# Performance work log

Hardware: AMD Instinct MI355X
Metric: run time of the kernel (lower is better)

## Reference

```python
import jax, jax.numpy as jnp
import numpy as np

H, C = 8, 640            # n_heads, sentence_size (per-head out channels)
HC = H * C               # 5120 concatenated head width
NS, NW, NSEC = 8192, 65536, 1024   # sentences, words, sections
EW, ES, ESEC = 131072, 262144, 16384
WORD, SENT, SECT = 300, 640, 512
FFN_HID = 2048


def setup_inputs() -> dict:
    key = jax.random.key(0)
    ks = jax.random.split(key, 32)
    f = lambda k, sh: (jax.random.normal(k, sh, jnp.float32) * 0.02)
    ri = jax.random.randint
    inp = {}
    inp['Hs'] = jax.random.normal(ks[0], (NS, SENT), jnp.float32)
    inp['Hw'] = jax.random.normal(ks[1], (NW, WORD), jnp.float32)
    inp['HS'] = jax.random.normal(ks[2], (NSEC, SECT), jnp.float32)
    # edge_index convention: row 0 = source nodes, row 1 = target (sentence) nodes
    inp['w2s'] = jnp.stack([ri(ks[3], (EW,), 0, NW), ri(ks[4], (EW,), 0, NS)]).astype(jnp.int32)
    inp['s2s'] = jnp.stack([ri(ks[5], (ES,), 0, NS), ri(ks[6], (ES,), 0, NS)]).astype(jnp.int32)
    inp['S2s'] = jnp.stack([ri(ks[7], (ESEC,), 0, NSEC), ri(ks[8], (ESEC,), 0, NS)]).astype(jnp.int32)
    # gat_w: bipartite (word -> sentence)
    inp['Ww_src'] = f(ks[9], (WORD, HC)); inp['Ww_dst'] = f(ks[10], (SENT, HC))
    inp['aw_src'] = f(ks[11], (H, C)); inp['aw_dst'] = f(ks[12], (H, C)); inp['bw'] = f(ks[13], (HC,))
    # gat_s: sentence -> sentence (shared lin for src/dst)
    inp['Ws'] = f(ks[14], (SENT, HC))
    inp['as_src'] = f(ks[15], (H, C)); inp['as_dst'] = f(ks[16], (H, C)); inp['bs'] = f(ks[17], (HC,))
    # gat_S: bipartite (section -> sentence)
    inp['WS_src'] = f(ks[18], (SECT, HC)); inp['WS_dst'] = f(ks[19], (SENT, HC))
    inp['aS_src'] = f(ks[20], (H, C)); inp['aS_dst'] = f(ks[21], (H, C)); inp['bS'] = f(ks[22], (HC,))
    # fusion gates
    inp['F1_w'] = f(ks[23], (2 * HC, HC)); inp['F1_b'] = f(ks[24], (HC,))
    inp['F2_w'] = f(ks[25], (2 * HC, HC)); inp['F2_b'] = f(ks[26], (HC,))
    # FFN
    inp['l1_w'] = f(ks[27], (HC, FFN_HID)); inp['l1_b'] = f(ks[28], (FFN_HID,))
    inp['l2_w'] = f(ks[29], (FFN_HID, SENT)); inp['l2_b'] = f(ks[30], (SENT,))
    return inp


def _gat(xs, xd, Wsrc, Wdst, asrc, adst, b, edge_index):
    """PyG-style GATConv (concat heads), bipartite (xs -> xd)."""
    N = xd.shape[0]
    hs = (xs @ Wsrc).reshape(-1, H, C)          # [Nsrc,H,C]
    hd = (xd @ Wdst).reshape(-1, H, C)          # [Ndst,H,C]
    al_s = jnp.einsum('nhc,hc->nh', hs, asrc)   # [Nsrc,H]
    al_d = jnp.einsum('nhc,hc->nh', hd, adst)   # [Ndst,H]
    src, dst = edge_index[0], edge_index[1]
    e = jax.nn.leaky_relu(al_s[src] + al_d[dst], negative_slope=0.2)  # [E,H]
    m = jax.ops.segment_max(e, dst, num_segments=N)                   # segment-stable softmax
    ex = jnp.exp(e - m[dst])
    den = jax.ops.segment_sum(ex, dst, num_segments=N)
    alpha = ex / (den[dst] + 1e-16)
    out = jax.ops.segment_sum(hs[src] * alpha[:, :, None], dst, num_segments=N)
    return out.reshape(N, HC) + b


def _fusion(X, Y, W, b):
    Z = jax.nn.sigmoid(jnp.concatenate([X, Y], axis=-1) @ W + b)
    return Z * X + (1.0 - Z) * Y


def reference(Hs, Hw, HS, w2s, s2s, S2s,
              Ww_src, Ww_dst, aw_src, aw_dst, bw,
              Ws, as_src, as_dst, bs,
              WS_src, WS_dst, aS_src, aS_dst, bS,
              F1_w, F1_b, F2_w, F2_b,
              l1_w, l1_b, l2_w, l2_b):
    Uw = jax.nn.elu(_gat(Hw, Hs, Ww_src, Ww_dst, aw_src, aw_dst, bw, w2s))
    Us = jax.nn.elu(_gat(Hs, Hs, Ws, Ws, as_src, as_dst, bs, s2s))
    US = jax.nn.elu(_gat(HS, Hs, WS_src, WS_dst, aS_src, aS_dst, bS, S2s))
    U1 = _fusion(Uw, Us, F1_w, F1_b)
    U2 = _fusion(U1, US, F2_w, F2_b)
    return (U2 @ l1_w + l1_b) @ l2_w + l2_b + Hs
```

## Files before the change

kernel.cpp:

```cpp
#include <hip/hip_runtime.h>
#include <cstdint>
#include <cstddef>

typedef __attribute__((ext_vector_type(8))) __bf16 bf16x8;
typedef __attribute__((ext_vector_type(4))) float f32x4;

static constexpr int kNS   = 8192;
static constexpr int kNW   = 65536;
static constexpr int kNSEC = 1024;
static constexpr int kEW   = 131072;
static constexpr int kES   = 262144;
static constexpr int kESEC = 16384;

__device__ __forceinline__ float eluf(float x)  { return x > 0.f ? x : (__expf(x) - 1.f); }
__device__ __forceinline__ float sigmf(float x) { return 1.f / (1.f + __expf(-x)); }

__device__ __forceinline__ void gload16(const __bf16* g, __bf16* l) {
  __builtin_amdgcn_global_load_lds((const __attribute__((address_space(1))) unsigned int*)g,
                                   (__attribute__((address_space(3))) unsigned int*)l,
                                   16, 0, 0);
}

__global__ __launch_bounds__(256) void conv_transpose(const float* __restrict__ W, int K, int N,
                                                      __bf16* __restrict__ Wt, int KP) {
  __shared__ float t[64][33];
  const int nb = blockIdx.x * 32, kb = blockIdx.y * 64;
  const int tx = threadIdx.x & 31, ty = threadIdx.x >> 5;
#pragma unroll
  for (int i = ty; i < 64; i += 8) {
    const int k = kb + i;
    t[i][tx] = (k < K) ? W[(long)k * N + nb + tx] : 0.f;
  }
  __syncthreads();
  union BU { __bf16 b; unsigned short u; };
#pragma unroll
  for (int i = ty; i < 32; i += 8) {
    BU b0, b1;
    b0.b = (__bf16)t[tx * 2][i];
    b1.b = (__bf16)t[tx * 2 + 1][i];
    const unsigned int pk = ((unsigned int)b1.u << 16) | b0.u;
    *(unsigned int*)(Wt + (long)(nb + i) * KP + kb + tx * 2) = pk;
  }
}

__global__ __launch_bounds__(256) void conv_bf(const float* __restrict__ in, __bf16* __restrict__ outb, long n) {
  long i = (long)blockIdx.x * blockDim.x + threadIdx.x;
  if (i < n) outb[i] = (__bf16)in[i];
}

__global__ __launch_bounds__(256) void head_vecs(const float* __restrict__ W, const float* __restrict__ a,
                                                 float* __restrict__ outv, int Kd, int KP) {
  const int h = blockIdx.x;
  const int lane = threadIdx.x & 63;
  const int k = blockIdx.y * 4 + (threadIdx.x >> 6);
  float s = 0.f;
  if (k < Kd) {
    const float* wr = W + (long)k * 5120 + h * 640;
    const float* ar = a + h * 640;
    for (int c = lane; c < 640; c += 64) s += wr[c] * ar[c];
  }
  for (int o2 = 32; o2; o2 >>= 1) s += __shfl_down(s, o2);
  if (lane == 0) outv[h * KP + k] = (k < Kd) ? s : 0.f;
}

__global__ __launch_bounds__(256) void comb_bias(const float* __restrict__ l1_b, const float* __restrict__ l2_w,
                                                 const float* __restrict__ l2_b, float* __restrict__ bc) {
  const int n = blockIdx.x * 256 + threadIdx.x;
  if (n >= 640) return;
  float s = l2_b[n];
  for (int k = 0; k < 2048; ++k) s += l1_b[k] * l2_w[(long)k * 640 + n];
  bc[n] = s;
}

__global__ __launch_bounds__(256) void att_logits(const float* __restrict__ X, int ldx, int Kd,
                                                  const float* __restrict__ vec, int KP,
                                                  float* __restrict__ outl, int N) {
  const int lane = threadIdx.x & 63;
  const int node = blockIdx.x * 4 + (threadIdx.x >> 6);
  if (node >= N) return;
  const float* xr = X + (long)node * ldx;
  float p[8];
#pragma unroll
  for (int h = 0; h < 8; ++h) p[h] = 0.f;
  for (int k = lane; k < Kd; k += 64) {
    const float xv = xr[k];
#pragma unroll
    for (int h = 0; h < 8; ++h) p[h] += xv * vec[h * KP + k];
  }
#pragma unroll
  for (int h = 0; h < 8; ++h) {
    float v = p[h];
    for (int o2 = 32; o2; o2 >>= 1) v += __shfl_down(v, o2);
    if (lane == 0) outl[(long)node * 8 + h] = v;
  }
}

__global__ __launch_bounds__(256) void att_logits4(const float* __restrict__ X,
                                                   const float* __restrict__ v0, const float* __restrict__ v1,
                                                   const float* __restrict__ v2, const float* __restrict__ v3,
                                                   float* __restrict__ o0, float* __restrict__ o1,
                                                   float* __restrict__ o2, float* __restrict__ o3, int N) {
  const int lane = threadIdx.x & 63;
  const int node = blockIdx.x * 4 + (threadIdx.x >> 6);
  if (node >= N) return;
  const float* xr = X + (long)node * 640;
  float p[4][8];
#pragma unroll
  for (int s = 0; s < 4; ++s)
#pragma unroll
    for (int h = 0; h < 8; ++h) p[s][h] = 0.f;
  for (int k = lane; k < 640; k += 64) {
    const float xv = xr[k];
#pragma unroll
    for (int h = 0; h < 8; ++h) {
      p[0][h] += xv * v0[h * 640 + k];
      p[1][h] += xv * v1[h * 640 + k];
      p[2][h] += xv * v2[h * 640 + k];
      p[3][h] += xv * v3[h * 640 + k];
    }
  }
  float* outs[4] = {o0, o1, o2, o3};
#pragma unroll
  for (int s = 0; s < 4; ++s)
#pragma unroll
    for (int h = 0; h < 8; ++h) {
      float v = p[s][h];
      for (int o2v = 32; o2v; o2v >>= 1) v += __shfl_down(v, o2v);
      if (lane == 0) outs[s][(long)node * 8 + h] = v;
    }
}

__global__ __launch_bounds__(256) void edge_count(const int* __restrict__ dst, int E, int* __restrict__ cnt) {
  const int gid = blockIdx.x * blockDim.x + threadIdx.x;
  if (gid < E) atomicAdd(&cnt[dst[gid]], 1);
}

__global__ __launch_bounds__(1024) void scan_off(const int* __restrict__ cnt, int* __restrict__ offo) {
  __shared__ int part[1024];
  const int tid = threadIdx.x;
  const int base = tid * 8;
  int loc[8];
  int s = 0;
#pragma unroll
  for (int i = 0; i < 8; ++i) { loc[i] = s; s += cnt[base + i]; }
  part[tid] = s;
  __syncthreads();
  for (int d2 = 1; d2 < 1024; d2 <<= 1) {
    int v = (tid >= d2) ? part[tid - d2] : 0;
    __syncthreads();
    part[tid] += v;
    __syncthreads();
  }
  const int pre = (tid > 0) ? part[tid - 1] : 0;
#pragma unroll
  for (int i = 0; i < 8; ++i) offo[base + i] = pre + loc[i];
  if (tid == 1023) offo[8192] = part[1023];
}

__global__ __launch_bounds__(256) void edge_fill(const int* __restrict__ src, const int* __restrict__ dst, int E,
                                                 const int* __restrict__ offo, int* __restrict__ cur,
                                                 int* __restrict__ ssrc) {
  const int gid = blockIdx.x * blockDim.x + threadIdx.x;
  if (gid < E) {
    const int d = dst[gid];
    const int p = offo[d] + atomicAdd(&cur[d], 1);
    ssrc[p] = src[gid];
  }
}

template <int FPAD, int F, bool XPH, bool BIASELU>
__global__ __launch_bounds__(256) void gat_agg(const int* __restrict__ seg_off, const int* __restrict__ ssrc,
                                               const float* __restrict__ als, const float* __restrict__ ald,
                                               const float* __restrict__ X, int ldx,
                                               __bf16* __restrict__ outp, int ldo,
                                               const float* __restrict__ bias) {
  constexpr int C4 = F / 4;
  constexpr int ITEMS = 8 * C4;
  constexpr int L = (ITEMS + 255) / 256;
  const int d = blockIdx.x;
  const int tid = threadIdx.x;
  const int o0 = seg_off[d], o1 = seg_off[d + 1];
  const int deg = o1 - o0;
  __shared__ float exl[64][8];
  __shared__ int ssl[64];
  __shared__ float aldd[8];
  __shared__ float den_s[8];
  if (tid < 8) { aldd[tid] = ald[(long)d * 8 + tid]; den_s[tid] = 0.f; }
  f32x4 acc[L];
  int hh[L], xo[L], oo[L];
  bool vld[L];
#pragma unroll
  for (int l = 0; l < L; ++l) {
    const int idx = tid + l * 256;
    vld[l] = (idx < ITEMS);
    const int h = vld[l] ? (idx / C4) : 0;
    const int c = vld[l] ? (idx - h * C4) : 0;
    hh[l] = h;
    xo[l] = (XPH ? h * F : 0) + c * 4;
    oo[l] = h * FPAD + c * 4;
#pragma unroll
    for (int r = 0; r < 4; ++r) acc[l][r] = 0.f;
  }
  __syncthreads();
  for (int base = 0; base < deg; base += 64) {
    const int nc = min(64, deg - base);
    if (tid < nc) ssl[tid] = ssrc[o0 + base + tid];
    __syncthreads();
    for (int t = tid; t < nc * 8; t += 256) {
      const int e = t >> 3, h = t & 7;
      float v = als[(long)ssl[e] * 8 + h] + aldd[h];
      v = v > 0.f ? v : 0.2f * v;
      exl[e][h] = __expf(v);
    }
    __syncthreads();
    if (tid < 8) {
      float s = 0.f;
      for (int e = 0; e < nc; ++e) s += exl[e][tid];
      den_s[tid] += s;
    }
    for (int e = 0; e < nc; ++e) {
      const float* xr = X + (long)ssl[e] * ldx;
      const float* ex8 = exl[e];
#pragma unroll
      for (int l = 0; l < L; ++l)
        if (vld[l]) {
          const f32x4 v = *(const f32x4*)(xr + xo[l]);
          acc[l] += ex8[hh[l]] * v;
        }
    }
    __syncthreads();
  }
#pragma unroll
  for (int l = 0; l < L; ++l) {
    if (!vld[l]) continue;
    const float dinv = 1.f / (den_s[hh[l]] + 1e-16f);
#pragma unroll
    for (int j = 0; j < 4; ++j) {
      float r = acc[l][j] * dinv;
      if constexpr (BIASELU) { r += bias[oo[l] + j]; r = eluf(r); }
      outp[(long)d * ldo + oo[l] + j] = (__bf16)r;
    }
  }
}

template <int EPI>
__global__ __launch_bounds__(256) void gemm_bt(
    const __bf16* __restrict__ A, int lda, const __bf16* __restrict__ A2, int ksplit,
    const __bf16* __restrict__ Bt, int ldb, int K,
    void* __restrict__ Cout, int ldc,
    const float* __restrict__ bias,
    const __bf16* __restrict__ Xg, const __bf16* __restrict__ Yg, int ldxy,
    const float* __restrict__ Res, int ldres,
    long a_zs, long bt_zs, long c_zs, int b_zs) {
  __shared__ __bf16 sA[2][128 * 32];
  __shared__ __bf16 sB[2][128 * 32];
  const int tid = threadIdx.x;
  const int z = blockIdx.z;
  const int m0 = blockIdx.y * 128, n0 = blockIdx.x * 128;
  const __bf16* Ab = A + (long)z * a_zs;
  const __bf16* A2b = A2 ? A2 + (long)z * a_zs : nullptr;
  const __bf16* Btb = Bt + (long)z * bt_zs;
  const int lane = tid & 63;
  const int wv = tid >> 6, wr = wv >> 1, wc = wv & 1;
  const int fr = lane & 15, fq = lane >> 4;

  const int r0 = tid >> 2, r1 = r0 + 64;
  const int csw = (((tid & 3) ^ ((r0 >> 1) & 3)) * 8);
  const int ldst0 = tid * 8;
  const int ldst1 = 2048 + tid * 8;

  f32x4 acc[4][4];
#pragma unroll
  for (int i = 0; i < 4; ++i)
#pragma unroll
    for (int j = 0; j < 4; ++j)
#pragma unroll
      for (int r = 0; r < 4; ++r) acc[i][j][r] = 0.f;

  const int fsw = (fq ^ ((fr >> 1) & 3)) * 8;
  int aof[4], bof[4];
#pragma unroll
  for (int i = 0; i < 4; ++i) {
    aof[i] = (wr * 64 + i * 16 + fr) * 32 + fsw;
    bof[i] = (wc * 64 + i * 16 + fr) * 32 + fsw;
  }

  const int nkt = K >> 5;
  auto stage = [&](int buf, int kt) {
    const int k0 = kt * 32;
    const __bf16* As = Ab;
    int kr = k0;
    if (A2b && k0 >= ksplit) { As = A2b; kr = k0 - ksplit; }
    gload16(As + (long)(m0 + r0) * lda + kr + csw, &sA[buf][ldst0]);
    gload16(As + (long)(m0 + r1) * lda + kr + csw, &sA[buf][ldst1]);
    gload16(Btb + (long)(n0 + r0) * ldb + k0 + csw, &sB[buf][ldst0]);
    gload16(Btb + (long)(n0 + r1) * ldb + k0 + csw, &sB[buf][ldst1]);
  };

  stage(0, 0);
  for (int kt = 0; kt < nkt; ++kt) {
    const int cur = kt & 1;
    __syncthreads();
    if (kt + 1 < nkt) stage(cur ^ 1, kt + 1);
    bf16x8 af[4], bfv[4];
#pragma unroll
    for (int i = 0; i < 4; ++i) {
      af[i] = *(const bf16x8*)(&sA[cur][aof[i]]);
      bfv[i] = *(const bf16x8*)(&sB[cur][bof[i]]);
    }
#pragma unroll
    for (int i = 0; i < 4; ++i)
#pragma unroll
      for (int j = 0; j < 4; ++j)
        acc[i][j] = __builtin_amdgcn_mfma_f32_16x16x32_bf16(af[i], bfv[j], acc[i][j], 0, 0, 0);
  }

  const float* biasb = bias ? bias + (long)z * b_zs : nullptr;
#pragma unroll
  for (int i = 0; i < 4; ++i) {
#pragma unroll
    for (int j = 0; j < 4; ++j) {
#pragma unroll
      for (int r = 0; r < 4; ++r) {
        const int mm = m0 + wr * 64 + i * 16 + fq * 4 + r;
        const int nn = n0 + wc * 64 + j * 16 + fr;
        const float v = acc[i][j][r];
        const long cidx = (long)mm * ldc + nn + (long)z * c_zs;
        if constexpr (EPI == 0) {
          ((float*)Cout)[cidx] = v;
        } else if constexpr (EPI == 1) {
          ((__bf16*)Cout)[cidx] = (__bf16)eluf(v + biasb[nn]);
        } else if constexpr (EPI == 2) {
          const float zt = sigmf(v + biasb[nn]);
          const float x = (float)Xg[(long)mm * ldxy + nn];
          const float y = (float)Yg[(long)mm * ldxy + nn];
          ((__bf16*)Cout)[cidx] = (__bf16)(zt * x + (1.f - zt) * y);
        } else if constexpr (EPI == 3) {
          ((__bf16*)Cout)[cidx] = (__bf16)(v + biasb[nn]);
        } else if constexpr (EPI == 4) {
          ((float*)Cout)[cidx] = v + biasb[nn] + Res[(long)mm * ldres + nn];
        } else {
          ((__bf16*)Cout)[cidx] = (__bf16)v;
        }
      }
    }
  }
}

template <int EPI>
__global__ __launch_bounds__(512, 2) void gemm256(
    const __bf16* __restrict__ A, int lda, const __bf16* __restrict__ A2, int ksplit,
    const __bf16* __restrict__ Bt, int ldb, int K,
    void* __restrict__ Cout, int ldc,
    const float* __restrict__ bias,
    const __bf16* __restrict__ Xg, const __bf16* __restrict__ Yg, int ldxy,
    int nn_tiles) {
  __shared__ __bf16 sA[2][2][256 * 32];
  __shared__ __bf16 sB[2][2][256 * 32];
  const int tid = threadIdx.x;

  const int nwg = gridDim.x;
  const int lin = blockIdx.x;
  const int qq = nwg >> 3, rr = nwg & 7;
  const int xcd = lin & 7, pos = lin >> 3;
  const int swz = (xcd < rr ? xcd * (qq + 1) : rr * (qq + 1) + (xcd - rr) * qq) + pos;
  const int m0 = (swz / nn_tiles) * 256;
  const int n0 = (swz % nn_tiles) * 256;

  const int lane = tid & 63;
  const int wv = tid >> 6, wm = wv >> 2, wn = wv & 3;
  const int fr = lane & 15, fq = lane >> 4;

  const int srow = tid >> 2;
  const int pslot = tid & 3;

  auto stageA = [&](int bp, int tt, int kk) {
    const int kcol0 = tt * 64 + kk * 32;
    const __bf16* src = A;
    int kc = kcol0;
    if (A2 && kcol0 >= ksplit) { src = A2; kc = kcol0 - ksplit; }
    __bf16* dst = &sA[bp][kk][0];
#pragma unroll
    for (int i = 0; i < 2; ++i) {
      const int r = i * 128 + srow;
      const int l = pslot ^ ((r >> 1) & 3);
      gload16(src + (long)(m0 + r) * lda + kc + l * 8, dst + (i * 512 + tid) * 8);
    }
  };
  auto stageB = [&](int bp, int tt, int kk) {
    const int kcol0 = tt * 64 + kk * 32;
    __bf16* dst = &sB[bp][kk][0];
#pragma unroll
    for (int i = 0; i < 2; ++i) {
      const int r = i * 128 + srow;
      const int l = pslot ^ ((r >> 1) & 3);
      gload16(Bt + (long)(n0 + r) * ldb + kcol0 + l * 8, dst + (i * 512 + tid) * 8);
    }
  };

  int aoff[8], boff[4];
#pragma unroll
  for (int mf = 0; mf < 8; ++mf) {
    const int ra = wm * 128 + mf * 16 + fr;
    aoff[mf] = ra * 32 + ((fq ^ ((ra >> 1) & 3)) * 8);
  }
#pragma unroll
  for (int nf = 0; nf < 4; ++nf) {
    const int rb = wn * 64 + nf * 16 + fr;
    boff[nf] = rb * 32 + ((fq ^ ((rb >> 1) & 3)) * 8);
  }

  f32x4 acc[8][4];
#pragma unroll
  for (int i = 0; i < 8; ++i)
#pragma unroll
    for (int j = 0; j < 4; ++j)
#pragma unroll
      for (int r = 0; r < 4; ++r) acc[i][j][r] = 0.f;

  const int nkt = K >> 6;

  stageA(0, 0, 0); stageB(0, 0, 0); stageA(0, 0, 1); stageB(0, 0, 1);
  asm volatile("s_waitcnt vmcnt(4)" ::: "memory");
  __builtin_amdgcn_s_barrier();

  for (int t = 0; t < nkt; ++t) {
    const int cb = t & 1, nb = cb ^ 1;
    const bool pf = (t + 1 < nkt);
    bf16x8 af[4], bfv[4];

#pragma unroll
    for (int mf = 0; mf < 4; ++mf) af[mf] = *(const bf16x8*)(&sA[cb][0][aoff[mf]]);
#pragma unroll
    for (int nf = 0; nf < 4; ++nf) bfv[nf] = *(const bf16x8*)(&sB[cb][0][boff[nf]]);
    if (pf) stageA(nb, t + 1, 0);
    __builtin_amdgcn_s_barrier();
    asm volatile("s_waitcnt lgkmcnt(0)" ::: "memory");
    __builtin_amdgcn_sched_barrier(0);
    __builtin_amdgcn_s_setprio(1);
#pragma unroll
    for (int mf = 0; mf < 4; ++mf)
#pragma unroll
      for (int nf = 0; nf < 4; ++nf)
        acc[mf][nf] = __builtin_amdgcn_mfma_f32_16x16x32_bf16(af[mf], bfv[nf], acc[mf][nf], 0, 0, 0);
    __builtin_amdgcn_s_setprio(0);

#pragma unroll
    for (int mf = 0; mf < 4; ++mf) af[mf] = *(const bf16x8*)(&sA[cb][0][aoff[4 + mf]]);
    if (pf) stageB(nb, t + 1, 0);
    if (pf) asm volatile("s_waitcnt vmcnt(4)" ::: "memory");
    else    asm volatile("s_waitcnt vmcnt(0)" ::: "memory");
    __builtin_amdgcn_s_barrier();
    asm volatile("s_waitcnt lgkmcnt(0)" ::: "memory");
    __builtin_amdgcn_sched_barrier(0);
    __builtin_amdgcn_s_setprio(1);
#pragma unroll
    for (int mf = 0; mf < 4; ++mf)
#pragma unroll
      for (int nf = 0; nf < 4; ++nf)
        acc[4 + mf][nf] = __builtin_amdgcn_mfma_f32_16x16x32_bf16(af[mf], bfv[nf], acc[4 + mf][nf], 0, 0, 0);
    __builtin_amdgcn_s_setprio(0);

#pragma unroll
    for (int mf = 0; mf < 4; ++mf) af[mf] = *(const bf16x8*)(&sA[cb][1][aoff[mf]]);
#pragma unroll
    for (int nf = 0; nf < 4; ++nf) bfv[nf] = *(const bf16x8*)(&sB[cb][1][boff[nf]]);
    if (pf) stageA(nb, t + 1, 1);
    __builtin_amdgcn_s_barrier();
    asm volatile("s_waitcnt lgkmcnt(0)" ::: "memory");
    __builtin_amdgcn_sched_barrier(0);
    __builtin_amdgcn_s_setprio(1);
#pragma unroll
    for (int mf = 0; mf < 4; ++mf)
#pragma unroll
      for (int nf = 0; nf < 4; ++nf)
        acc[mf][nf] = __builtin_amdgcn_mfma_f32_16x16x32_bf16(af[mf], bfv[nf], acc[mf][nf], 0, 0, 0);
    __builtin_amdgcn_s_setprio(0);

#pragma unroll
    for (int mf = 0; mf < 4; ++mf) af[mf] = *(const bf16x8*)(&sA[cb][1][aoff[4 + mf]]);
    if (pf) {
      stageB(nb, t + 1, 1);
      asm volatile("s_waitcnt vmcnt(4)" ::: "memory");
    }
    __builtin_amdgcn_s_barrier();
    asm volatile("s_waitcnt lgkmcnt(0)" ::: "memory");
    __builtin_amdgcn_sched_barrier(0);
    __builtin_amdgcn_s_setprio(1);
#pragma unroll
    for (int mf = 0; mf < 4; ++mf)
#pragma unroll
      for (int nf = 0; nf < 4; ++nf)
        acc[4 + mf][nf] = __builtin_amdgcn_mfma_f32_16x16x32_bf16(af[mf], bfv[nf], acc[4 + mf][nf], 0, 0, 0);
    __builtin_amdgcn_s_setprio(0);
  }

#pragma unroll
  for (int mf = 0; mf < 8; ++mf) {
#pragma unroll
    for (int nf = 0; nf < 4; ++nf) {
#pragma unroll
      for (int r = 0; r < 4; ++r) {
        const int mm = m0 + wm * 128 + mf * 16 + fq * 4 + r;
        const int nn = n0 + wn * 64 + nf * 16 + fr;
        const float v = acc[mf][nf][r];
        const long cidx = (long)mm * ldc + nn;
        if constexpr (EPI == 2) {
          const float zt = sigmf(v + bias[nn]);
          const float x = (float)Xg[(long)mm * ldxy + nn];
          const float y = (float)Yg[(long)mm * ldxy + nn];
          ((__bf16*)Cout)[cidx] = (__bf16)(zt * x + (1.f - zt) * y);
        } else {
          ((__bf16*)Cout)[cidx] = (__bf16)(v + bias[nn]);
        }
      }
    }
  }
}

extern "C" void kernel_launch(void* const* d_in, const int* in_sizes, int n_in,
                              void* d_out, int out_size, void* d_ws, size_t ws_size,
                              hipStream_t stream) {
  (void)in_sizes; (void)n_in; (void)out_size; (void)ws_size;
  const float* Hs    = (const float*)d_in[0];
  const float* Hw    = (const float*)d_in[1];
  const float* HSec  = (const float*)d_in[2];
  const int* w2s     = (const int*)d_in[3];
  const int* s2s     = (const int*)d_in[4];
  const int* S2s     = (const int*)d_in[5];
  const float* Ww_src = (const float*)d_in[6];
  const float* Ww_dst = (const float*)d_in[7];
  const float* aw_src = (const float*)d_in[8];
  const float* aw_dst = (const float*)d_in[9];
  const float* bw     = (const float*)d_in[10];
  const float* Wss    = (const float*)d_in[11];
  const float* as_src = (const float*)d_in[12];
  const float* as_dst = (const float*)d_in[13];
  const float* bs     = (const float*)d_in[14];
  const float* WS_src = (const float*)d_in[15];
  const float* WS_dst = (const float*)d_in[16];
  const float* aS_src = (const float*)d_in[17];
  const float* aS_dst = (const float*)d_in[18];
  const float* bS     = (const float*)d_in[19];
  const float* F1_w   = (const float*)d_in[20];
  const float* F1_b   = (const float*)d_in[21];
  const float* F2_w   = (const float*)d_in[22];
  const float* F2_b   = (const float*)d_in[23];
  const float* l1_w   = (const float*)d_in[24];
  const float* l1_b   = (const float*)d_in[25];
  const float* l2_w   = (const float*)d_in[26];
  const float* l2_b   = (const float*)d_in[27];
  float* outp = (float*)d_out;

  char* ws = (char*)d_ws;
  size_t cur_off = 0;
  auto alloc = [&](size_t bytes) -> char* {
    char* p = ws + cur_off;
    cur_off = (cur_off + bytes + 255) & ~(size_t)255;
    return p;
  };

  __bf16* Wt_w  = (__bf16*)alloc((size_t)5120 * 320 * 2);
  __bf16* Wt_s  = (__bf16*)alloc((size_t)5120 * 640 * 2);
  __bf16* Wt_S  = (__bf16*)alloc((size_t)5120 * 512 * 2);
  __bf16* WtF   = (__bf16*)alloc((size_t)5120 * 10240 * 2);
  __bf16* Wt_l2 = (__bf16*)alloc((size_t)640 * 2048 * 2);
  __bf16* l1_bf = (__bf16*)alloc((size_t)5120 * 2048 * 2);
  __bf16* WcT   = (__bf16*)alloc((size_t)640 * 5120 * 2);
  float*  bc    = (float*)alloc(640 * 4);
  __bf16* HS_bf = (__bf16*)alloc((size_t)1024 * 512 * 2);
  float* v_w = (float*)alloc(8 * 320 * 4);
  float* u_w = (float*)alloc(8 * 640 * 4);
  float* v_s = (float*)alloc(8 * 640 * 4);
  float* u_s = (float*)alloc(8 * 640 * 4);
  float* v_S = (float*)alloc(8 * 512 * 4);
  float* u_S = (float*)alloc(8 * 640 * 4);
  float* alw_s = (float*)alloc((size_t)kNW * 8 * 4);
  float* alw_d = (float*)alloc((size_t)kNS * 8 * 4);
  float* als_s = (float*)alloc((size_t)kNS * 8 * 4);
  float* als_d = (float*)alloc((size_t)kNS * 8 * 4);
  float* alS_s = (float*)alloc((size_t)kNSEC * 8 * 4);
  float* alS_d = (float*)alloc((size_t)kNS * 8 * 4);
  int* csr_i  = (int*)alloc((size_t)6 * kNS * 4);
  int* cnt_w = csr_i, *cnt_s = csr_i + kNS, *cnt_S = csr_i + 2 * kNS;
  int* cur_w = csr_i + 3 * kNS, *cur_s = csr_i + 4 * kNS, *cur_S = csr_i + 5 * kNS;
  int* off_w = (int*)alloc((size_t)(kNS + 1) * 4);
  int* off_s = (int*)alloc((size_t)(kNS + 1) * 4);
  int* off_S = (int*)alloc((size_t)(kNS + 1) * 4);
  int* ssrc_w = (int*)alloc((size_t)kEW * 4);
  int* ssrc_s = (int*)alloc((size_t)kES * 4);
  int* ssrc_S = (int*)alloc((size_t)kESEC * 4);
  float* hs_S = (float*)alloc((size_t)1024 * 5120 * 4);
  char* aggreg = alloc((size_t)kNS * 2560 * 2 + (size_t)kNS * 5120 * 2);
  __bf16* agg_w = (__bf16*)aggreg;
  __bf16* agg_s = (__bf16*)(aggreg + (size_t)kNS * 2560 * 2);
  __bf16* U1 = (__bf16*)aggreg;
  __bf16* Uw = (__bf16*)alloc((size_t)kNS * 5120 * 2);
  __bf16* Us = (__bf16*)alloc((size_t)kNS * 5120 * 2);
  __bf16* US = (__bf16*)alloc((size_t)kNS * 5120 * 2);
  __bf16* U2 = Uw;

  const dim3 b256(256);

  conv_transpose<<<dim3(160, 5), b256, 0, stream>>>(Ww_src, 300, 5120, Wt_w, 320);
  conv_transpose<<<dim3(160, 10), b256, 0, stream>>>(Wss, 640, 5120, Wt_s, 640);
  conv_transpose<<<dim3(160, 8), b256, 0, stream>>>(WS_src, 512, 5120, Wt_S, 512);
  conv_transpose<<<dim3(160, 160), b256, 0, stream>>>(F1_w, 10240, 5120, WtF, 10240);
  conv_transpose<<<dim3(20, 32), b256, 0, stream>>>(l2_w, 2048, 640, Wt_l2, 2048);
  conv_bf<<<(1024 * 512 + 255) / 256, b256, 0, stream>>>(HSec, HS_bf, (long)1024 * 512);
  conv_bf<<<((long)5120 * 2048 + 255) / 256, b256, 0, stream>>>(l1_w, l1_bf, (long)5120 * 2048);

  gemm_bt<5><<<dim3(40, 5, 1), b256, 0, stream>>>(
      Wt_l2, 2048, nullptr, 1 << 30, l1_bf, 2048, 2048,
      WcT, 5120, nullptr, nullptr, nullptr, 0, nullptr, 0, 0, 0, 0, 0);
  comb_bias<<<3, b256, 0, stream>>>(l1_b, l2_w, l2_b, bc);

  head_vecs<<<dim3(8, 80), b256, 0, stream>>>(Ww_src, aw_src, v_w, 300, 320);
  head_vecs<<<dim3(8, 160), b256, 0, stream>>>(Ww_dst, aw_dst, u_w, 640, 640);
  head_vecs<<<dim3(8, 160), b256, 0, stream>>>(Wss, as_src, v_s, 640, 640);
  head_vecs<<<dim3(8, 160), b256, 0, stream>>>(Wss, as_dst, u_s, 640, 640);
  head_vecs<<<dim3(8, 128), b256, 0, stream>>>(WS_src, aS_src, v_S, 512, 512);
  head_vecs<<<dim3(8, 160), b256, 0, stream>>>(WS_dst, aS_dst, u_S, 640, 640);

  att_logits<<<(kNW + 3) / 4, b256, 0, stream>>>(Hw, 300, 300, v_w, 320, alw_s, kNW);
  att_logits<<<(kNSEC + 3) / 4, b256, 0, stream>>>(HSec, 512, 512, v_S, 512, alS_s, kNSEC);
  att_logits4<<<(kNS + 3) / 4, b256, 0, stream>>>(Hs, u_w, v_s, u_s, u_S,
                                                  alw_d, als_s, als_d, alS_d, kNS);

  hipMemsetAsync(csr_i, 0, (size_t)6 * kNS * 4, stream);
  edge_count<<<(kEW + 255) / 256, b256, 0, stream>>>(w2s + kEW, kEW, cnt_w);
  edge_count<<<(kES + 255) / 256, b256, 0, stream>>>(s2s + kES, kES, cnt_s);
  edge_count<<<(kESEC + 255) / 256, b256, 0, stream>>>(S2s + kESEC, kESEC, cnt_S);
  scan_off<<<1, 1024, 0, stream>>>(cnt_w, off_w);
  scan_off<<<1, 1024, 0, stream>>>(cnt_s, off_s);
  scan_off<<<1, 1024, 0, stream>>>(cnt_S, off_S);
  edge_fill<<<(kEW + 255) / 256, b256, 0, stream>>>(w2s, w2s + kEW, kEW, off_w, cur_w, ssrc_w);
  edge_fill<<<(kES + 255) / 256, b256, 0, stream>>>(s2s, s2s + kES, kES, off_s, cur_s, ssrc_s);
  edge_fill<<<(kESEC + 255) / 256, b256, 0, stream>>>(S2s, S2s + kESEC, kESEC, off_S, cur_S, ssrc_S);

  gemm_bt<0><<<dim3(40, 8, 1), b256, 0, stream>>>(
      HS_bf, 512, nullptr, 1 << 30, Wt_S, 512, 512,
      hs_S, 5120, nullptr, nullptr, nullptr, 0, nullptr, 0, 0, 0, 0, 0);

  gat_agg<320, 300, false, false><<<kNS, b256, 0, stream>>>(off_w, ssrc_w, alw_s, alw_d, Hw, 300, agg_w, 2560, nullptr);
  gat_agg<640, 640, false, false><<<kNS, b256, 0, stream>>>(off_s, ssrc_s, als_s, als_d, Hs, 640, agg_s, 5120, nullptr);
  gat_agg<640, 640, true, true><<<kNS, b256, 0, stream>>>(off_S, ssrc_S, alS_s, alS_d, hs_S, 5120, US, 5120, bS);

  gemm_bt<1><<<dim3(5, 64, 8), b256, 0, stream>>>(
      agg_w, 2560, nullptr, 1 << 30, Wt_w, 320, 320,
      Uw, 5120, bw, nullptr, nullptr, 0, nullptr, 0, 320, (long)640 * 320, 640, 640);
  gemm_bt<1><<<dim3(5, 64, 8), b256, 0, stream>>>(
      agg_s, 5120, nullptr, 1 << 30, Wt_s, 640, 640,
      Us, 5120, bs, nullptr, nullptr, 0, nullptr, 0, 640, (long)640 * 640, 640, 640);

  gemm256<2><<<dim3(640), dim3(512), 0, stream>>>(
      Uw, 5120, Us, 5120, WtF, 10240, 10240,
      U1, 5120, F1_b, Uw, Us, 5120, 20);

  conv_transpose<<<dim3(160, 160), b256, 0, stream>>>(F2_w, 10240, 5120, WtF, 10240);
  gemm256<2><<<dim3(640), dim3(512), 0, stream>>>(
      U1, 5120, US, 5120, WtF, 10240, 10240,
      U2, 5120, F2_b, U1, US, 5120, 20);

  gemm_bt<4><<<dim3(5, 64, 1), b256, 0, stream>>>(
      U2, 5120, nullptr, 1 << 30, WcT, 5120, 5120,
      outp, 640, bc, nullptr, nullptr, 0, Hs, 640, 0, 0, 0, 0);
}
```

Before: 3.139 ms.

## Double-buffer MFMA fragment registers to overlap LDS reads with compute

```diff
diff --git a/kernel.cpp b/kernel.cpp
--- a/kernel.cpp
+++ b/kernel.cpp
@@ -420,79 +420,92 @@
 
   const int nkt = K >> 6;
 
+  bf16x8 aA[4], aB[4], bA[4], bB[4];
+
   stageA(0, 0, 0); stageB(0, 0, 0); stageA(0, 0, 1); stageB(0, 0, 1);
   asm volatile("s_waitcnt vmcnt(4)" ::: "memory");
   __builtin_amdgcn_s_barrier();
+#pragma unroll
+  for (int mf = 0; mf < 4; ++mf) aA[mf] = *(const bf16x8*)(&sA[0][0][aoff[mf]]);
+#pragma unroll
+  for (int nf = 0; nf < 4; ++nf) bA[nf] = *(const bf16x8*)(&sB[0][0][boff[nf]]);
 
   for (int t = 0; t < nkt; ++t) {
     const int cb = t & 1, nb = cb ^ 1;
     const bool pf = (t + 1 < nkt);
-    bf16x8 af[4], bfv[4];
-
-#pragma unroll
-    for (int mf = 0; mf < 4; ++mf) af[mf] = *(const bf16x8*)(&sA[cb][0][aoff[mf]]);
-#pragma unroll
-    for (int nf = 0; nf < 4; ++nf) bfv[nf] = *(const bf16x8*)(&sB[cb][0][boff[nf]]);
+
+#pragma unroll
+    for (int mf = 0; mf < 4; ++mf) aB[mf] = *(const bf16x8*)(&sA[cb][0][aoff[4 + mf]]);
     if (pf) stageA(nb, t + 1, 0);
-    __builtin_amdgcn_s_barrier();
-    asm volatile("s_waitcnt lgkmcnt(0)" ::: "memory");
+    asm volatile("s_waitcnt lgkmcnt(4)" ::: "memory");
     __builtin_amdgcn_sched_barrier(0);
     __builtin_amdgcn_s_setprio(1);
 #pragma unroll
     for (int mf = 0; mf < 4; ++mf)
 #pragma unroll
       for (int nf = 0; nf < 4; ++nf)
-        acc[mf][nf] = __builtin_amdgcn_mfma_f32_16x16x32_bf16(af[mf], bfv[nf], acc[mf][nf], 0, 0, 0);
+        acc[mf][nf] = __builtin_amdgcn_mfma_f32_16x16x32_bf16(aA[mf], bA[nf], acc[mf][nf], 0, 0, 0);
     __builtin_amdgcn_s_setprio(0);
-
-#pragma unroll
-    for (int mf = 0; mf < 4; ++mf) af[mf] = *(const bf16x8*)(&sA[cb][0][aoff[4 + mf]]);
+    __builtin_amdgcn_sched_barrier(0);
+
     if (pf) stageB(nb, t + 1, 0);
     if (pf) asm volatile("s_waitcnt vmcnt(4)" ::: "memory");
     else    asm volatile("s_waitcnt vmcnt(0)" ::: "memory");
     __builtin_amdgcn_s_barrier();
-    asm volatile("s_waitcnt lgkmcnt(0)" ::: "memory");
+
+#pragma unroll
+    for (int mf = 0; mf < 4; ++mf) aA[mf] = *(const bf16x8*)(&sA[cb][1][aoff[mf]]);
+#pragma unroll
+    for (int nf = 0; nf < 4; ++nf) bB[nf] = *(const bf16x8*)(&sB[cb][1][boff[nf]]);
+    asm volatile("s_waitcnt lgkmcnt(8)" ::: "memory");
     __builtin_amdgcn_sched_barrier(0);
     __builtin_amdgcn_s_setprio(1);
 #pragma unroll
     for (int mf = 0; mf < 4; ++mf)
 #pragma unroll
       for (int nf = 0; nf < 4; ++nf)
-        acc[4 + mf][nf] = __builtin_amdgcn_mfma_f32_16x16x32_bf16(af[mf], bfv[nf], acc[4 + mf][nf], 0, 0, 0);
+        acc[4 + mf][nf] = __builtin_amdgcn_mfma_f32_16x16x32_bf16(aB[mf], bA[nf], acc[4 + mf][nf], 0, 0, 0);
     __builtin_amdgcn_s_setprio(0);
-
-#pragma unroll
-    for (int mf = 0; mf < 4; ++mf) af[mf] = *(const bf16x8*)(&sA[cb][1][aoff[mf]]);
-#pragma unroll
-    for (int nf = 0; nf < 4; ++nf) bfv[nf] = *(const bf16x8*)(&sB[cb][1][boff[nf]]);
+    __builtin_amdgcn_sched_barrier(0);
+
+#pragma unroll
+    for (int mf = 0; mf < 4; ++mf) aB[mf] = *(const bf16x8*)(&sA[cb][1][aoff[4 + mf]]);
     if (pf) stageA(nb, t + 1, 1);
-    __builtin_amdgcn_s_barrier();
-    asm volatile("s_waitcnt lgkmcnt(0)" ::: "memory");
+    asm volatile("s_waitcnt lgkmcnt(4)" ::: "memory");
     __builtin_amdgcn_sched_barrier(0);
     __builtin_amdgcn_s_setprio(1);
 #pragma unroll
     for (int mf = 0; mf < 4; ++mf)
 #pragma unroll
       for (int nf = 0; nf < 4; ++nf)
-        acc[mf][nf] = __builtin_amdgcn_mfma_f32_16x16x32_bf16(af[mf], bfv[nf], acc[mf][nf], 0, 0, 0);
+        acc[mf][nf] = __builtin_amdgcn_mfma_f32_16x16x32_bf16(aA[mf], bB[nf], acc[mf][nf], 0, 0, 0);
     __builtin_amdgcn_s_setprio(0);
-
-#pragma unroll
-    for (int mf = 0; mf < 4; ++mf) af[mf] = *(const bf16x8*)(&sA[cb][1][aoff[4 + mf]]);
+    __builtin_amdgcn_sched_barrier(0);
+
     if (pf) {
       stageB(nb, t + 1, 1);
       asm volatile("s_waitcnt vmcnt(4)" ::: "memory");
     }
     __builtin_amdgcn_s_barrier();
-    asm volatile("s_waitcnt lgkmcnt(0)" ::: "memory");
+
+    if (pf) {
+#pragma unroll
+      for (int mf = 0; mf < 4; ++mf) aA[mf] = *(const bf16x8*)(&sA[nb][0][aoff[mf]]);
+#pragma unroll
+      for (int nf = 0; nf < 4; ++nf) bA[nf] = *(const bf16x8*)(&sB[nb][0][boff[nf]]);
+      asm volatile("s_waitcnt lgkmcnt(8)" ::: "memory");
+    } else {
+      asm volatile("s_waitcnt lgkmcnt(0)" ::: "memory");
+    }
     __builtin_amdgcn_sched_barrier(0);
     __builtin_amdgcn_s_setprio(1);
 #pragma unroll
     for (int mf = 0; mf < 4; ++mf)
 #pragma unroll
       for (int nf = 0; nf < 4; ++nf)
-        acc[4 + mf][nf] = __builtin_amdgcn_mfma_f32_16x16x32_bf16(af[mf], bfv[nf], acc[4 + mf][nf], 0, 0, 0);
+        acc[4 + mf][nf] = __builtin_amdgcn_mfma_f32_16x16x32_bf16(aB[mf], bB[nf], acc[4 + mf][nf], 0, 0, 0);
     __builtin_amdgcn_s_setprio(0);
+    __builtin_amdgcn_sched_barrier(0);
   }
 
 #pragma unroll
```

Result: no change. 3.089 ms (-1.6%).
